# Performance work log

Hardware: AMD Instinct MI355X
Metric: run time of the kernel (lower is better)

Reference implementation:

```python
import jax, jax.numpy as jnp
import numpy as np

N_NODES = 65536
N_EDGES = 1048576
DIM = 64  # in_dim == out_dim == pooling kernel size


def setup_inputs() -> dict:
    key = jax.random.key(0)
    ks = jax.random.split(key, 6)
    s = 1.0 / np.sqrt(DIM)
    return {
        "x": jax.random.normal(ks[0], (N_NODES, DIM), dtype=jnp.float32),
        "edge_index": jax.random.randint(ks[1], (2, N_EDGES), 0, N_NODES, dtype=jnp.int32),
        "edge_weight": jax.random.uniform(ks[2], (N_EDGES,), dtype=jnp.float32),
        "W1": jax.random.normal(ks[3], (DIM, DIM), dtype=jnp.float32) * s,
        "b1": jnp.zeros((DIM,), dtype=jnp.float32),
        "W2": jax.random.normal(ks[4], (DIM, DIM), dtype=jnp.float32) * s,
        "b2": jnp.zeros((DIM,), dtype=jnp.float32),
    }


def gcn_conv(x, edge_index, edge_weight, W, b):
    """PyG GCNConv: symmetric-normalized aggregation with implicit self-loops (weight 1)."""
    n = x.shape[0]
    row, col = edge_index[0], edge_index[1]  # messages flow row -> col
    # degree includes self-loop weight 1
    deg = jnp.zeros((n,), dtype=x.dtype).at[col].add(edge_weight) + 1.0
    dinv = jnp.where(deg > 0, jax.lax.rsqrt(deg), 0.0)
    norm = dinv[row] * edge_weight * dinv[col]  # [E]
    h = x @ W  # linear transform first (no bias, bias added after aggregation)
    out = jnp.zeros_like(h).at[col].add(norm[:, None] * h[row])
    # self-loop message: norm = dinv[i]*1*dinv[i]
    out = out + h * (dinv * dinv)[:, None]
    return out + b


def reference(x, edge_index, edge_weight, W1, b1, W2, b2):
    h = gcn_conv(x, edge_index, edge_weight, W1, b1)
    h = gcn_conv(h, edge_index, edge_weight, W2, b2)  # [N, D]
    # AvgPool1d(kernel=D) over node axis of [1, D, N]: windows of D nodes, stride D
    n, d = h.shape
    m = n // d  # number of full windows
    pooled = h[: m * d].reshape(m, d, d).mean(axis=1)  # [M, D]
    return pooled.T  # squeeze -> [D, M]
```

## Files before the change

### kernel.cpp

```cpp
#include <hip/hip_runtime.h>

#define N_NODES 65536
#define N_EDGES 1048576
#define DIM 64
#define M_POOL (N_NODES / DIM)
#define NCOARSE 256
#define SEGCAP 5120
#define P3CHUNK 4096
#define P3BLOCKS (N_EDGES / P3CHUNK)
#define GEMM_BLOCKS 1024
#define FUSED_BLOCKS (GEMM_BLOCKS + P3BLOCKS)

typedef unsigned int u32;
typedef unsigned short u16;

__device__ __forceinline__ float bf2f(u32 hi16) {
    return __uint_as_float(hi16 << 16);
}
__device__ __forceinline__ u32 f2bf(float f) {
    u32 u = __float_as_uint(f);
    return (u + 0x7fffu + ((u >> 16) & 1u)) >> 16;
}


__global__ __launch_bounds__(256) void zero_cursor(int* __restrict__ cursor) {
    cursor[threadIdx.x] = 0;
}


__global__ __launch_bounds__(1024) void fused_gemm_p3(const float* __restrict__ x,
                                                      const float* __restrict__ W,
                                                      u16* __restrict__ hb,
                                                      const int* __restrict__ col,
                                                      const int* __restrict__ row,
                                                      const float* __restrict__ ew,
                                                      int* __restrict__ cursor,
                                                      int2* __restrict__ csr_tmp) {
    __shared__ __align__(16) char sm[52224];
    const int t = threadIdx.x;
    const int b = blockIdx.x;

    if ((b % 5) == 4) {
        int2* stg      = (int2*)sm;
        int*  gpA      = (int*)(sm + 32768);
        int*  h2       = (int*)(sm + 49152);
        int*  off      = (int*)(sm + 50176);
        int*  base_blk = (int*)(sm + 51200);
        const int e0 = (b / 5) * P3CHUNK + t * 4;

        if (t < NCOARSE) h2[t] = 0;
        __syncthreads();

        const int4 c4 = *(const int4*)&col[e0];
        const int4 r4 = *(const int4*)&row[e0];
        const float4 w4 = *(const float4*)&ew[e0];
        const int cc[4] = {c4.x >> 8, c4.y >> 8, c4.z >> 8, c4.w >> 8};

        atomicAdd(&h2[cc[0]], 1);
        atomicAdd(&h2[cc[1]], 1);
        atomicAdd(&h2[cc[2]], 1);
        atomicAdd(&h2[cc[3]], 1);
        __syncthreads();

        const int myc = (t < NCOARSE) ? h2[t] : 0;
        if (t < NCOARSE) off[t] = myc;
        __syncthreads();
        for (int o = 1; o < NCOARSE; o <<= 1) {
            int v = 0;
            if (t < NCOARSE && t >= o) v = off[t - o];
            __syncthreads();
            if (t < NCOARSE) off[t] += v;
            __syncthreads();
        }
        if (t < NCOARSE) {
            off[t] -= myc;
            base_blk[t] = myc ? atomicAdd(&cursor[t], myc) : 0;
            h2[t] = 0;
        }
        __syncthreads();

        const int fi[4] = {c4.x & 255, c4.y & 255, c4.z & 255, c4.w & 255};
        const int rr[4] = {r4.x, r4.y, r4.z, r4.w};
        const float wv[4] = {w4.x, w4.y, w4.z, w4.w};
#pragma unroll
        for (int j = 0; j < 4; ++j) {
            const int c = cc[j];
            const int r = atomicAdd(&h2[c], 1);
            const int s = off[c] + r;
            const int bp = base_blk[c] + r;
            stg[s] = make_int2((rr[j] << 8) | fi[j], __float_as_int(wv[j]));
            gpA[s] = (bp < SEGCAP) ? (c * SEGCAP + bp) : -1;
        }
        __syncthreads();
        for (int i = t; i < P3CHUNK; i += 1024) {
            const int gp = gpA[i];
            if (gp >= 0) csr_tmp[gp] = stg[i];
        }
    } else {
        float* Ws = (float*)sm;
        float* Xs = (float*)(sm + 16384);
        const int row0 = (b - b / 5) * 64;
        for (int i = t; i < DIM * DIM; i += 1024) Ws[i] = W[i];
        for (int i = t; i < 64 * DIM; i += 1024)
            Xs[i] = x[(size_t)row0 * DIM + i];
        __syncthreads();
        const int j = t & 63;
        const int rs = t >> 6;
        for (int rrr = 0; rrr < 4; ++rrr) {
            const int r = rs * 4 + rrr;
            float acc = 0.f;
#pragma unroll
            for (int k = 0; k < DIM; ++k) acc += Xs[r * DIM + k] * Ws[k * DIM + j];
            hb[(size_t)(row0 + r) * DIM + j] = (u16)f2bf(acc);
        }
    }
}


__global__ __launch_bounds__(512) void p4_fine(const int* __restrict__ cursor,
                                               const int2* __restrict__ csr_tmp,
                                               u32* __restrict__ csr,
                                               int* __restrict__ rowptr,
                                               float* __restrict__ dinv,
                                               u16* __restrict__ hb) {
    __shared__ int2 A[SEGCAP];
    __shared__ u32 Bu[SEGCAP];
    __shared__ int fh[NCOARSE];
    __shared__ int off2[NCOARSE];
    __shared__ int cbase[NCOARSE];
    __shared__ float degw[NCOARSE];
    __shared__ float dvs[NCOARSE];
    const int t = threadIdx.x;
    const int c = blockIdx.x;
    const int segN = min(cursor[c], SEGCAP);

    if (t < NCOARSE) cbase[t] = min(cursor[t], SEGCAP);
    __syncthreads();
    for (int o = 1; o < NCOARSE; o <<= 1) {
        int v = 0;
        if (t < NCOARSE && t >= o) v = cbase[t - o];
        __syncthreads();
        if (t < NCOARSE) cbase[t] += v;
        __syncthreads();
    }
    const int seg0_out = cbase[c] - segN;

    for (int i = t; i < segN; i += 512) A[i] = csr_tmp[c * SEGCAP + i];
    if (t < NCOARSE) { fh[t] = 0; degw[t] = 0.f; }
    __syncthreads();

    for (int i = t; i < segN; i += 512) {
        const int f = A[i].x & 255;
        atomicAdd(&fh[f], 1);
        atomicAdd(&degw[f], __int_as_float(A[i].y));
    }
    __syncthreads();

    if (t < NCOARSE) off2[t] = fh[t];
    __syncthreads();
    for (int o = 1; o < NCOARSE; o <<= 1) {
        int v = 0;
        if (t < NCOARSE && t >= o) v = off2[t - o];
        __syncthreads();
        if (t < NCOARSE) off2[t] += v;
        __syncthreads();
    }
    if (t < NCOARSE) {
        off2[t] -= fh[t];
        const float dv = rsqrtf(1.0f + degw[t]);
        dvs[t] = dv;
        dinv[c * 256 + t] = dv;
        rowptr[c * 256 + t] = seg0_out + off2[t];
        fh[t] = 0;
    }
    if (c == NCOARSE - 1 && t == 0) rowptr[N_NODES] = seg0_out + segN;
    __syncthreads();

    for (int idx = t; idx < 256 * 8; idx += 512) {
        const int nl = idx >> 3;
        const int part = idx & 7;
        const float dv = dvs[nl];
        const size_t p = (size_t)(c * 256 + nl) * DIM + part * 8;
        uint4 v = *(const uint4*)&hb[p];
        uint4 o;
        o.x = f2bf(dv * bf2f(v.x & 0xffff)) | (f2bf(dv * bf2f(v.x >> 16)) << 16);
        o.y = f2bf(dv * bf2f(v.y & 0xffff)) | (f2bf(dv * bf2f(v.y >> 16)) << 16);
        o.z = f2bf(dv * bf2f(v.z & 0xffff)) | (f2bf(dv * bf2f(v.z >> 16)) << 16);
        o.w = f2bf(dv * bf2f(v.w & 0xffff)) | (f2bf(dv * bf2f(v.w >> 16)) << 16);
        *(uint4*)&hb[p] = o;
    }

    for (int i = t; i < segN; i += 512) {
        const int f = A[i].x & 255;
        const int r = atomicAdd(&fh[f], 1);
        const float w = __int_as_float(A[i].y) * dvs[f];
        Bu[off2[f] + r] = (f2bf(w) << 16) | ((u32)(A[i].x >> 8) & 0xffffu);
    }
    __syncthreads();
    for (int i = t; i < segN; i += 512)
        csr[seg0_out + i] = Bu[i];
}


__global__ __launch_bounds__(256) void aggregate_l1(const int* __restrict__ rowptr,
                                                    const u32* __restrict__ csr,
                                                    const u16* __restrict__ hb2,
                                                    const float* __restrict__ dinv,
                                                    const float* __restrict__ bias,
                                                    u16* __restrict__ ob) {
    const int lane = threadIdx.x & 63;
    const int node = (blockIdx.x * 256 + threadIdx.x) >> 6;
    const int g = lane >> 3;
    const int q = lane & 7;
    const int start = rowptr[node];
    const int end = rowptr[node + 1];
    const float dv = dinv[node];

    float acc[8];
#pragma unroll
    for (int k = 0; k < 8; ++k) acc[k] = 0.f;

    for (int i = start; i < end; i += 16) {
        const int i0 = i + g;
        const int i1 = i + 8 + g;
        const u32 v0 = (i0 < end) ? csr[i0] : 0;
        const u32 v1 = (i1 < end) ? csr[i1] : 0;
        const float w0 = bf2f(v0 >> 16);
        const float w1 = bf2f(v1 >> 16);
        const uint4 B0 = *(const uint4*)&hb2[(size_t)(v0 & 0xffffu) * DIM + q * 8];
        const uint4 B1 = *(const uint4*)&hb2[(size_t)(v1 & 0xffffu) * DIM + q * 8];
        acc[0] += w0 * bf2f(B0.x & 0xffff) + w1 * bf2f(B1.x & 0xffff);
        acc[1] += w0 * bf2f(B0.x >> 16)    + w1 * bf2f(B1.x >> 16);
        acc[2] += w0 * bf2f(B0.y & 0xffff) + w1 * bf2f(B1.y & 0xffff);
        acc[3] += w0 * bf2f(B0.y >> 16)    + w1 * bf2f(B1.y >> 16);
        acc[4] += w0 * bf2f(B0.z & 0xffff) + w1 * bf2f(B1.z & 0xffff);
        acc[5] += w0 * bf2f(B0.z >> 16)    + w1 * bf2f(B1.z >> 16);
        acc[6] += w0 * bf2f(B0.w & 0xffff) + w1 * bf2f(B1.w & 0xffff);
        acc[7] += w0 * bf2f(B0.w >> 16)    + w1 * bf2f(B1.w >> 16);
    }
#pragma unroll
    for (int m = 8; m <= 32; m <<= 1) {
#pragma unroll
        for (int k = 0; k < 8; ++k) acc[k] += __shfl_xor(acc[k], m, 64);
    }
    if (lane < 8) {
        const uint4 S = *(const uint4*)&hb2[(size_t)node * DIM + q * 8];
        float r[8];
        r[0] = dv * (acc[0] + dv * bf2f(S.x & 0xffff) + bias[q * 8 + 0]);
        r[1] = dv * (acc[1] + dv * bf2f(S.x >> 16)    + bias[q * 8 + 1]);
        r[2] = dv * (acc[2] + dv * bf2f(S.y & 0xffff) + bias[q * 8 + 2]);
        r[3] = dv * (acc[3] + dv * bf2f(S.y >> 16)    + bias[q * 8 + 3]);
        r[4] = dv * (acc[4] + dv * bf2f(S.z & 0xffff) + bias[q * 8 + 4]);
        r[5] = dv * (acc[5] + dv * bf2f(S.z >> 16)    + bias[q * 8 + 5]);
        r[6] = dv * (acc[6] + dv * bf2f(S.w & 0xffff) + bias[q * 8 + 6]);
        r[7] = dv * (acc[7] + dv * bf2f(S.w >> 16)    + bias[q * 8 + 7]);
        uint4 o;
        o.x = f2bf(r[0]) | (f2bf(r[1]) << 16);
        o.y = f2bf(r[2]) | (f2bf(r[3]) << 16);
        o.z = f2bf(r[4]) | (f2bf(r[5]) << 16);
        o.w = f2bf(r[6]) | (f2bf(r[7]) << 16);
        *(uint4*)&ob[(size_t)node * DIM + q * 8] = o;
    }
}


__global__ __launch_bounds__(512) void agg2_pool_gemm(const int* __restrict__ rowptr,
                                                      const u32* __restrict__ csr,
                                                      const u16* __restrict__ hb,
                                                      const float* __restrict__ dinv,
                                                      const float* __restrict__ W2,
                                                      const float* __restrict__ b2,
                                                      float* __restrict__ out) {
    __shared__ float Ws[DIM * DIM];
    __shared__ float wacc[8][DIM];
    __shared__ float pooled[DIM];
    const int t = threadIdx.x;
    const int m = blockIdx.x;

    for (int i = t; i < DIM * DIM; i += 512) Ws[i] = W2[i];

    const int wave = t >> 6;
    const int lane = t & 63;
    const int g = lane >> 3;
    const int q = lane & 7;

    const int start = rowptr[m * 64];
    const int end = rowptr[m * 64 + 64];

    float acc[8];
#pragma unroll
    for (int k = 0; k < 8; ++k) acc[k] = 0.f;

    for (int i = start + wave * 32; i < end; i += 256) {
        const int i0 = i + g;
        const int i1 = i + 8 + g;
        const int i2 = i + 16 + g;
        const int i3 = i + 24 + g;
        const u32 v0 = (i0 < end) ? csr[i0] : 0;
        const u32 v1 = (i1 < end) ? csr[i1] : 0;
        const u32 v2 = (i2 < end) ? csr[i2] : 0;
        const u32 v3 = (i3 < end) ? csr[i3] : 0;
        const float w0 = bf2f(v0 >> 16);
        const float w1 = bf2f(v1 >> 16);
        const float w2 = bf2f(v2 >> 16);
        const float w3 = bf2f(v3 >> 16);
        const uint4 B0 = *(const uint4*)&hb[(size_t)(v0 & 0xffffu) * DIM + q * 8];
        const uint4 B1 = *(const uint4*)&hb[(size_t)(v1 & 0xffffu) * DIM + q * 8];
        const uint4 B2 = *(const uint4*)&hb[(size_t)(v2 & 0xffffu) * DIM + q * 8];
        const uint4 B3 = *(const uint4*)&hb[(size_t)(v3 & 0xffffu) * DIM + q * 8];
        acc[0] += w0 * bf2f(B0.x & 0xffff) + w1 * bf2f(B1.x & 0xffff)
                + w2 * bf2f(B2.x & 0xffff) + w3 * bf2f(B3.x & 0xffff);
        acc[1] += w0 * bf2f(B0.x >> 16)    + w1 * bf2f(B1.x >> 16)
                + w2 * bf2f(B2.x >> 16)    + w3 * bf2f(B3.x >> 16);
        acc[2] += w0 * bf2f(B0.y & 0xffff) + w1 * bf2f(B1.y & 0xffff)
                + w2 * bf2f(B2.y & 0xffff) + w3 * bf2f(B3.y & 0xffff);
        acc[3] += w0 * bf2f(B0.y >> 16)    + w1 * bf2f(B1.y >> 16)
                + w2 * bf2f(B2.y >> 16)    + w3 * bf2f(B3.y >> 16);
        acc[4] += w0 * bf2f(B0.z & 0xffff) + w1 * bf2f(B1.z & 0xffff)
                + w2 * bf2f(B2.z & 0xffff) + w3 * bf2f(B3.z & 0xffff);
        acc[5] += w0 * bf2f(B0.z >> 16)    + w1 * bf2f(B1.z >> 16)
                + w2 * bf2f(B2.z >> 16)    + w3 * bf2f(B3.z >> 16);
        acc[6] += w0 * bf2f(B0.w & 0xffff) + w1 * bf2f(B1.w & 0xffff)
                + w2 * bf2f(B2.w & 0xffff) + w3 * bf2f(B3.w & 0xffff);
        acc[7] += w0 * bf2f(B0.w >> 16)    + w1 * bf2f(B1.w >> 16)
                + w2 * bf2f(B2.w >> 16)    + w3 * bf2f(B3.w >> 16);
    }

    {
        const int node = m * 64 + wave * 8 + g;
        const float dv = dinv[node];
        const uint4 S = *(const uint4*)&hb[(size_t)node * DIM + q * 8];
        acc[0] += dv * bf2f(S.x & 0xffff);
        acc[1] += dv * bf2f(S.x >> 16);
        acc[2] += dv * bf2f(S.y & 0xffff);
        acc[3] += dv * bf2f(S.y >> 16);
        acc[4] += dv * bf2f(S.z & 0xffff);
        acc[5] += dv * bf2f(S.z >> 16);
        acc[6] += dv * bf2f(S.w & 0xffff);
        acc[7] += dv * bf2f(S.w >> 16);
    }

#pragma unroll
    for (int mm = 8; mm <= 32; mm <<= 1) {
#pragma unroll
        for (int k = 0; k < 8; ++k) acc[k] += __shfl_xor(acc[k], mm, 64);
    }
    if (lane < 8) {
#pragma unroll
        for (int k = 0; k < 8; ++k) wacc[wave][q * 8 + k] = acc[k];
    }
    __syncthreads();
    if (t < DIM) {
        float p = 0.f;
#pragma unroll
        for (int w = 0; w < 8; ++w) p += wacc[w][t];
        pooled[t] = p * (1.0f / DIM);
    }
    __syncthreads();
    if (t < DIM) {
        float o = b2[t];
#pragma unroll
        for (int k = 0; k < DIM; ++k) o += pooled[k] * Ws[k * DIM + t];
        out[(size_t)t * M_POOL + m] = o;
    }
}


extern "C" void kernel_launch(void* const* d_in, const int* in_sizes, int n_in,
                              void* d_out, int out_size, void* d_ws, size_t ws_size,
                              hipStream_t stream) {
    const float* x  = (const float*)d_in[0];
    const int*   ei = (const int*)d_in[1];
    const float* ew = (const float*)d_in[2];
    const float* W1 = (const float*)d_in[3];
    const float* b1 = (const float*)d_in[4];
    const float* W2 = (const float*)d_in[5];
    const float* b2 = (const float*)d_in[6];
    float* out = (float*)d_out;

    char* w = (char*)d_ws;
    int*   cursor = (int*)w;   w += 1024;
    int*   rowptr = (int*)w;   w += (size_t)(N_NODES + 16) * 4;
    float* dinv   = (float*)w; w += (size_t)N_NODES * 4;
    int2*  csrt   = (int2*)w;  w += (size_t)NCOARSE * SEGCAP * 8;
    u32*   csr    = (u32*)w;   w += (size_t)N_EDGES * 4;
    u16*   hbf    = (u16*)w;   w += (size_t)N_NODES * DIM * 2;
    u16*   h1bf   = (u16*)w;

    const int* row = ei;
    const int* col = ei + N_EDGES;

    zero_cursor<<<1, 256, 0, stream>>>(cursor);
    fused_gemm_p3<<<FUSED_BLOCKS, 1024, 0, stream>>>(x, W1, hbf, col, row, ew,
                                                     cursor, csrt);
    p4_fine<<<NCOARSE, 512, 0, stream>>>(cursor, csrt, csr, rowptr, dinv, hbf);

    aggregate_l1<<<N_NODES / 4, 256, 0, stream>>>(rowptr, csr, hbf, dinv, b1, h1bf);

    agg2_pool_gemm<<<M_POOL, 512, 0, stream>>>(rowptr, csr, h1bf, dinv, W2, b2, out);
}
```

Measured before the change: 121.3 us.

## Use wavefront shuffle scans and halve edge-binning chunk size

```diff
diff --git a/kernel.cpp b/kernel.cpp
--- a/kernel.cpp
+++ b/kernel.cpp
@@ -6,7 +6,7 @@
 #define M_POOL (N_NODES / DIM)
 #define NCOARSE 256
 #define SEGCAP 5120
-#define P3CHUNK 4096
+#define P3CHUNK 2048
 #define P3BLOCKS (N_EDGES / P3CHUNK)
 #define GEMM_BLOCKS 1024
 #define FUSED_BLOCKS (GEMM_BLOCKS + P3BLOCKS)
@@ -20,6 +20,30 @@
 __device__ __forceinline__ u32 f2bf(float f) {
     u32 u = __float_as_uint(f);
     return (u + 0x7fffu + ((u >> 16) & 1u)) >> 16;
+}
+
+__device__ __forceinline__ void scan256_wave(int* arr, int* wsum, int t) {
+    int s = 0;
+    if (t < 256) {
+        s = arr[t];
+        const int lane = t & 63;
+#pragma unroll
+        for (int o = 1; o < 64; o <<= 1) {
+            const int u = __shfl_up(s, o, 64);
+            if (lane >= o) s += u;
+        }
+        if (lane == 63) wsum[t >> 6] = s;
+    }
+    __syncthreads();
+    if (t < 256) {
+        const int w = t >> 6;
+        int add = 0;
+#pragma unroll
+        for (int k = 0; k < 4; ++k)
+            if (k < w) add += wsum[k];
+        arr[t] = s + add;
+    }
+    __syncthreads();
 }
 
 
@@ -36,42 +60,35 @@
                                                       const float* __restrict__ ew,
                                                       int* __restrict__ cursor,
                                                       int2* __restrict__ csr_tmp) {
-    __shared__ __align__(16) char sm[52224];
+    __shared__ __align__(16) char sm[33280];
     const int t = threadIdx.x;
     const int b = blockIdx.x;
 
-    if ((b % 5) == 4) {
+    if ((b % 3) == 2) {
         int2* stg      = (int2*)sm;
-        int*  gpA      = (int*)(sm + 32768);
-        int*  h2       = (int*)(sm + 49152);
-        int*  off      = (int*)(sm + 50176);
-        int*  base_blk = (int*)(sm + 51200);
-        const int e0 = (b / 5) * P3CHUNK + t * 4;
+        int*  gpA      = (int*)(sm + 16384);
+        int*  h2       = (int*)(sm + 24576);
+        int*  off      = (int*)(sm + 25600);
+        int*  base_blk = (int*)(sm + 26624);
+        int*  wsum     = (int*)(sm + 27648);
+        const int e0 = (b / 3) * P3CHUNK + t * 2;
 
         if (t < NCOARSE) h2[t] = 0;
         __syncthreads();
 
-        const int4 c4 = *(const int4*)&col[e0];
-        const int4 r4 = *(const int4*)&row[e0];
-        const float4 w4 = *(const float4*)&ew[e0];
-        const int cc[4] = {c4.x >> 8, c4.y >> 8, c4.z >> 8, c4.w >> 8};
+        const int2 c2 = *(const int2*)&col[e0];
+        const int2 r2 = *(const int2*)&row[e0];
+        const float2 w2 = *(const float2*)&ew[e0];
+        const int cc[2] = {c2.x >> 8, c2.y >> 8};
 
         atomicAdd(&h2[cc[0]], 1);
         atomicAdd(&h2[cc[1]], 1);
-        atomicAdd(&h2[cc[2]], 1);
-        atomicAdd(&h2[cc[3]], 1);
         __syncthreads();
 
         const int myc = (t < NCOARSE) ? h2[t] : 0;
         if (t < NCOARSE) off[t] = myc;
         __syncthreads();
-        for (int o = 1; o < NCOARSE; o <<= 1) {
-            int v = 0;
-            if (t < NCOARSE && t >= o) v = off[t - o];
-            __syncthreads();
-            if (t < NCOARSE) off[t] += v;
-            __syncthreads();
-        }
+        scan256_wave(off, wsum, t);
         if (t < NCOARSE) {
             off[t] -= myc;
             base_blk[t] = myc ? atomicAdd(&cursor[t], myc) : 0;
@@ -79,11 +96,11 @@
         }
         __syncthreads();
 
-        const int fi[4] = {c4.x & 255, c4.y & 255, c4.z & 255, c4.w & 255};
-        const int rr[4] = {r4.x, r4.y, r4.z, r4.w};
-        const float wv[4] = {w4.x, w4.y, w4.z, w4.w};
-#pragma unroll
-        for (int j = 0; j < 4; ++j) {
+        const int fi[2] = {c2.x & 255, c2.y & 255};
+        const int rr[2] = {r2.x, r2.y};
+        const float wv[2] = {w2.x, w2.y};
+#pragma unroll
+        for (int j = 0; j < 2; ++j) {
             const int c = cc[j];
             const int r = atomicAdd(&h2[c], 1);
             const int s = off[c] + r;
@@ -99,7 +116,7 @@
     } else {
         float* Ws = (float*)sm;
         float* Xs = (float*)(sm + 16384);
-        const int row0 = (b - b / 5) * 64;
+        const int row0 = (b - b / 3) * 64;
         for (int i = t; i < DIM * DIM; i += 1024) Ws[i] = W[i];
         for (int i = t; i < 64 * DIM; i += 1024)
             Xs[i] = x[(size_t)row0 * DIM + i];
@@ -130,19 +147,14 @@
     __shared__ int cbase[NCOARSE];
     __shared__ float degw[NCOARSE];
     __shared__ float dvs[NCOARSE];
+    __shared__ int wsum[4];
     const int t = threadIdx.x;
     const int c = blockIdx.x;
     const int segN = min(cursor[c], SEGCAP);
 
     if (t < NCOARSE) cbase[t] = min(cursor[t], SEGCAP);
     __syncthreads();
-    for (int o = 1; o < NCOARSE; o <<= 1) {
-        int v = 0;
-        if (t < NCOARSE && t >= o) v = cbase[t - o];
-        __syncthreads();
-        if (t < NCOARSE) cbase[t] += v;
-        __syncthreads();
-    }
+    scan256_wave(cbase, wsum, t);
     const int seg0_out = cbase[c] - segN;
 
     for (int i = t; i < segN; i += 512) A[i] = csr_tmp[c * SEGCAP + i];
@@ -158,13 +170,7 @@
 
     if (t < NCOARSE) off2[t] = fh[t];
     __syncthreads();
-    for (int o = 1; o < NCOARSE; o <<= 1) {
-        int v = 0;
-        if (t < NCOARSE && t >= o) v = off2[t - o];
-        __syncthreads();
-        if (t < NCOARSE) off2[t] += v;
-        __syncthreads();
-    }
+    scan256_wave(off2, wsum, t);
     if (t < NCOARSE) {
         off2[t] -= fh[t];
         const float dv = rsqrtf(1.0f + degw[t]);
```

Measured after the change: 123.6 us. No clear change (+1.9%).
